# Kernel tuning notes

Hardware: AMD Instinct MI355X
Metric: run time of the kernel (lower is better)

The kernel has to match this reference:

```python
import jax, jax.numpy as jnp
import numpy as np

B, T, D = 32, 2048, 512

def setup_inputs() -> dict:
    key = jax.random.key(0)
    x = jax.random.normal(key, (B, T, D), dtype=jnp.float32)
    return {"x": x}

def reference(x) -> jnp.ndarray:
    # w[b,t] = sum_s <x_bt, x_bs> - <x_bt, x_bt>
    # Equivalent to x_bt . (sum_s x_bs) - ||x_bt||^2; avoids the [B,T,T] matrix.
    s = x.sum(axis=1)                                  # [B, D]
    w = jnp.einsum('btd,bd->bt', x, s) - (x * x).sum(axis=-1)  # [B, T]
    weights = jax.nn.softmax(w, axis=1)                # softmax over time
    # weighted pooling over time -> [B, D]
    representations = jnp.einsum('btd,bt->bd', x, weights)
    return representations
```

## Files before the change

kernel.cpp:

```cpp
#include <hip/hip_runtime.h>
#include <math.h>

constexpr int B = 32;
constexpr int T = 2048;
constexpr int D = 512;

constexpr int C1 = 32;
constexpr int R1 = T / C1;
constexpr int C2 = 128;
constexpr int RW = 4;
constexpr int NPART = C2;

__global__ __launch_bounds__(256) void colsum_part(const float* __restrict__ x,
                                                   float* __restrict__ P1) {
    const int b = blockIdx.x, c = blockIdx.y;
    const int d4 = threadIdx.x & 127;
    const int rp = threadIdx.x >> 7;
    const float4* xp = (const float4*)x + ((size_t)(b * T + c * R1) * D >> 2)
                       + (size_t)rp * (D / 4) + d4;
    float4 acc = {0.f, 0.f, 0.f, 0.f};
    #pragma unroll 8
    for (int i = 0; i < R1 / 2; ++i) {
        float4 v = xp[(size_t)i * (D / 2)];
        acc.x += v.x; acc.y += v.y; acc.z += v.z; acc.w += v.w;
    }
    __shared__ float4 lds[128];
    if (rp == 1) lds[d4] = acc;
    __syncthreads();
    if (rp == 0) {
        float4 o = lds[d4];
        acc.x += o.x; acc.y += o.y; acc.z += o.z; acc.w += o.w;
        ((float4*)P1)[(size_t)(b * C1 + c) * (D / 4) + d4] = acc;
    }
}

__global__ __launch_bounds__(256) void fused_pool(const float* __restrict__ x,
                                                  const float* __restrict__ P1,
                                                  float* __restrict__ Mp,
                                                  float* __restrict__ Sp,
                                                  float* __restrict__ Op) {
    const int b = blockIdx.x, c = blockIdx.y;
    const int tid = threadIdx.x, wid = tid >> 6, lane = tid & 63;

    __shared__ float  s_lds[D];
    __shared__ float  mred[4], sred[4];
    __shared__ float4 Obuf[4][D / 4];

    const int t0 = c * (4 * RW) + wid * RW;
    const float4* xr = (const float4*)(x + ((size_t)b * T + t0) * D) + lane * 2;
    float4 X0[RW], X1[RW];
    #pragma unroll
    for (int r = 0; r < RW; ++r) { X0[r] = xr[0]; X1[r] = xr[1]; xr += D / 4; }

    {
        const float2* pp = (const float2*)(P1 + (size_t)b * C1 * D) + tid;
        float2 acc = {0.f, 0.f};
        #pragma unroll
        for (int k = 0; k < C1; ++k) {
            float2 v = pp[(size_t)k * (D / 2)];
            acc.x += v.x; acc.y += v.y;
        }
        ((float2*)s_lds)[tid] = acc;
    }
    __syncthreads();
    const float4 s0 = ((const float4*)s_lds)[lane * 2];
    const float4 s1 = ((const float4*)s_lds)[lane * 2 + 1];

    float a[RW];
    #pragma unroll
    for (int r = 0; r < RW; ++r) {
        float t;
        t =      X0[r].x * (s0.x - X0[r].x);
        t = fmaf(X0[r].y,  s0.y - X0[r].y, t);
        t = fmaf(X0[r].z,  s0.z - X0[r].z, t);
        t = fmaf(X0[r].w,  s0.w - X0[r].w, t);
        t = fmaf(X1[r].x,  s1.x - X1[r].x, t);
        t = fmaf(X1[r].y,  s1.y - X1[r].y, t);
        t = fmaf(X1[r].z,  s1.z - X1[r].z, t);
        t = fmaf(X1[r].w,  s1.w - X1[r].w, t);
        a[r] = t;
    }
    #pragma unroll
    for (int off = 1; off < 64; off <<= 1) {
        #pragma unroll
        for (int r = 0; r < RW; ++r) a[r] += __shfl_xor(a[r], off, 64);
    }

    float m = fmaxf(fmaxf(a[0], a[1]), fmaxf(a[2], a[3]));
    float e[RW], ssum = 0.f;
    #pragma unroll
    for (int r = 0; r < RW; ++r) { e[r] = __expf(a[r] - m); ssum += e[r]; }

    float4 O0 = {0.f,0.f,0.f,0.f}, O1 = {0.f,0.f,0.f,0.f};
    #pragma unroll
    for (int r = 0; r < RW; ++r) {
        O0.x = fmaf(e[r], X0[r].x, O0.x); O0.y = fmaf(e[r], X0[r].y, O0.y);
        O0.z = fmaf(e[r], X0[r].z, O0.z); O0.w = fmaf(e[r], X0[r].w, O0.w);
        O1.x = fmaf(e[r], X1[r].x, O1.x); O1.y = fmaf(e[r], X1[r].y, O1.y);
        O1.z = fmaf(e[r], X1[r].z, O1.z); O1.w = fmaf(e[r], X1[r].w, O1.w);
    }

    if (lane == 0) { mred[wid] = m; sred[wid] = ssum; }
    __syncthreads();
    const float Mb = fmaxf(fmaxf(mred[0], mred[1]), fmaxf(mred[2], mred[3]));
    const float fw = __expf(m - Mb);
    Obuf[wid][lane * 2]     = make_float4(O0.x * fw, O0.y * fw, O0.z * fw, O0.w * fw);
    Obuf[wid][lane * 2 + 1] = make_float4(O1.x * fw, O1.y * fw, O1.z * fw, O1.w * fw);
    __syncthreads();
    if (tid == 0) {
        float Sb = sred[0] * __expf(mred[0] - Mb) + sred[1] * __expf(mred[1] - Mb)
                 + sred[2] * __expf(mred[2] - Mb) + sred[3] * __expf(mred[3] - Mb);
        Mp[b * C2 + c] = Mb;
        Sp[b * C2 + c] = Sb;
    }
    if (tid < D / 4) {
        float4 v0 = Obuf[0][tid], v1 = Obuf[1][tid], v2 = Obuf[2][tid], v3 = Obuf[3][tid];
        float4 r;
        r.x = (v0.x + v1.x) + (v2.x + v3.x);
        r.y = (v0.y + v1.y) + (v2.y + v3.y);
        r.z = (v0.z + v1.z) + (v2.z + v3.z);
        r.w = (v0.w + v1.w) + (v2.w + v3.w);
        ((float4*)Op)[(size_t)(b * C2 + c) * (D / 4) + tid] = r;
    }
}

__global__ __launch_bounds__(256) void merge_out(const float* __restrict__ Mp,
                                                 const float* __restrict__ Sp,
                                                 const float* __restrict__ Op,
                                                 float* __restrict__ out) {
    const int b = blockIdx.x;
    const int tid = threadIdx.x, wid = tid >> 6, lane = tid & 63;
    __shared__ float fmerge[NPART];
    __shared__ float red[4];
    __shared__ float misc[1];

    float Mc = -INFINITY, Sc = 0.f;
    if (tid < NPART) { Mc = Mp[b * NPART + tid]; Sc = Sp[b * NPART + tid]; }

    float mm = Mc;
    #pragma unroll
    for (int off = 1; off < 64; off <<= 1) mm = fmaxf(mm, __shfl_xor(mm, off, 64));
    if (lane == 0) red[wid] = mm;
    __syncthreads();
    const float Mg = fmaxf(fmaxf(red[0], red[1]), fmaxf(red[2], red[3]));
    __syncthreads();

    const float f = __expf(Mc - Mg);
    if (tid < NPART) fmerge[tid] = f;
    float fs = f * Sc;
    #pragma unroll
    for (int off = 1; off < 64; off <<= 1) fs += __shfl_xor(fs, off, 64);
    if (lane == 0) red[wid] = fs;
    __syncthreads();
    if (tid == 0) misc[0] = 1.0f / (red[0] + red[1] + red[2] + red[3]);
    __syncthreads();
    const float inv = misc[0];

    float2 acc = {0.f, 0.f};
    const float2* op = (const float2*)Op + (size_t)b * NPART * (D / 2) + tid;
    #pragma unroll 8
    for (int cc = 0; cc < NPART; ++cc) {
        const float fc = fmerge[cc];
        float2 v = op[(size_t)cc * (D / 2)];
        acc.x = fmaf(fc, v.x, acc.x);
        acc.y = fmaf(fc, v.y, acc.y);
    }
    ((float2*)out)[(size_t)b * (D / 2) + tid] = make_float2(acc.x * inv, acc.y * inv);
}

extern "C" void kernel_launch(void* const* d_in, const int* in_sizes, int n_in,
                              void* d_out, int out_size, void* d_ws, size_t ws_size,
                              hipStream_t stream) {
    const float* x = (const float*)d_in[0];
    float* out = (float*)d_out;

    float* P1 = (float*)d_ws;
    float* Mp = P1 + (size_t)B * C1 * D;
    float* Sp = Mp + (size_t)B * C2;
    float* Op = Sp + (size_t)B * C2;

    colsum_part<<<dim3(B, C1), 256, 0, stream>>>(x, P1);
    fused_pool<<<dim3(B, C2), 256, 0, stream>>>(x, P1, Mp, Sp, Op);
    merge_out<<<B, 256, 0, stream>>>(Mp, Sp, Op, out);
}
```

Baseline: 223.0 us.

## Process multiple row chunks per block with online softmax and register prefetch

Each wave now loops over several 4-row chunks and keeps a running max, sum and weighted accumulator in online-softmax style. The next chunk's rows are prefetched into registers while the current one is processed. Block count per batch drops by four, which reduces partial outputs, the redundant column-sum reduction per block and the merge work. The trade-off is fewer blocks in flight and a serial dependence across chunks, which could limit memory parallelism.

```diff
diff --git a/kernel.cpp b/kernel.cpp
--- a/kernel.cpp
+++ b/kernel.cpp
@@ -7,8 +7,10 @@
 
 constexpr int C1 = 32;
 constexpr int R1 = T / C1;
-constexpr int C2 = 128;
+constexpr int C2 = 32;
+constexpr int RPB = T / C2;
 constexpr int RW = 4;
+constexpr int NCHUNK = RPB / (4 * RW);
 constexpr int NPART = C2;
 
 __global__ __launch_bounds__(256) void colsum_part(const float* __restrict__ x,
@@ -46,7 +48,7 @@
     __shared__ float  mred[4], sred[4];
     __shared__ float4 Obuf[4][D / 4];
 
-    const int t0 = c * (4 * RW) + wid * RW;
+    const int t0 = c * RPB + wid * (NCHUNK * RW);
     const float4* xr = (const float4*)(x + ((size_t)b * T + t0) * D) + lane * 2;
     float4 X0[RW], X1[RW];
     #pragma unroll
@@ -66,38 +68,56 @@
     const float4 s0 = ((const float4*)s_lds)[lane * 2];
     const float4 s1 = ((const float4*)s_lds)[lane * 2 + 1];
 
-    float a[RW];
-    #pragma unroll
-    for (int r = 0; r < RW; ++r) {
-        float t;
-        t =      X0[r].x * (s0.x - X0[r].x);
-        t = fmaf(X0[r].y,  s0.y - X0[r].y, t);
-        t = fmaf(X0[r].z,  s0.z - X0[r].z, t);
-        t = fmaf(X0[r].w,  s0.w - X0[r].w, t);
-        t = fmaf(X1[r].x,  s1.x - X1[r].x, t);
-        t = fmaf(X1[r].y,  s1.y - X1[r].y, t);
-        t = fmaf(X1[r].z,  s1.z - X1[r].z, t);
-        t = fmaf(X1[r].w,  s1.w - X1[r].w, t);
-        a[r] = t;
-    }
-    #pragma unroll
-    for (int off = 1; off < 64; off <<= 1) {
-        #pragma unroll
-        for (int r = 0; r < RW; ++r) a[r] += __shfl_xor(a[r], off, 64);
-    }
-
-    float m = fmaxf(fmaxf(a[0], a[1]), fmaxf(a[2], a[3]));
-    float e[RW], ssum = 0.f;
-    #pragma unroll
-    for (int r = 0; r < RW; ++r) { e[r] = __expf(a[r] - m); ssum += e[r]; }
-
+    float m = -INFINITY, ssum = 0.f;
     float4 O0 = {0.f,0.f,0.f,0.f}, O1 = {0.f,0.f,0.f,0.f};
-    #pragma unroll
-    for (int r = 0; r < RW; ++r) {
-        O0.x = fmaf(e[r], X0[r].x, O0.x); O0.y = fmaf(e[r], X0[r].y, O0.y);
-        O0.z = fmaf(e[r], X0[r].z, O0.z); O0.w = fmaf(e[r], X0[r].w, O0.w);
-        O1.x = fmaf(e[r], X1[r].x, O1.x); O1.y = fmaf(e[r], X1[r].y, O1.y);
-        O1.z = fmaf(e[r], X1[r].z, O1.z); O1.w = fmaf(e[r], X1[r].w, O1.w);
+
+    #pragma unroll
+    for (int ch = 0; ch < NCHUNK; ++ch) {
+        float4 Y0[RW], Y1[RW];
+        #pragma unroll
+        for (int r = 0; r < RW; ++r) { Y0[r] = X0[r]; Y1[r] = X1[r]; }
+        if (ch + 1 < NCHUNK) {
+            #pragma unroll
+            for (int r = 0; r < RW; ++r) { X0[r] = xr[0]; X1[r] = xr[1]; xr += D / 4; }
+        }
+
+        float a[RW];
+        #pragma unroll
+        for (int r = 0; r < RW; ++r) {
+            float t;
+            t =      Y0[r].x * (s0.x - Y0[r].x);
+            t = fmaf(Y0[r].y,  s0.y - Y0[r].y, t);
+            t = fmaf(Y0[r].z,  s0.z - Y0[r].z, t);
+            t = fmaf(Y0[r].w,  s0.w - Y0[r].w, t);
+            t = fmaf(Y1[r].x,  s1.x - Y1[r].x, t);
+            t = fmaf(Y1[r].y,  s1.y - Y1[r].y, t);
+            t = fmaf(Y1[r].z,  s1.z - Y1[r].z, t);
+            t = fmaf(Y1[r].w,  s1.w - Y1[r].w, t);
+            a[r] = t;
+        }
+        #pragma unroll
+        for (int off = 1; off < 64; off <<= 1) {
+            #pragma unroll
+            for (int r = 0; r < RW; ++r) a[r] += __shfl_xor(a[r], off, 64);
+        }
+
+        const float mc = fmaxf(fmaxf(a[0], a[1]), fmaxf(a[2], a[3]));
+        const float mn = fmaxf(m, mc);
+        const float f  = __expf(m - mn);
+        float e[RW], es = 0.f;
+        #pragma unroll
+        for (int r = 0; r < RW; ++r) { e[r] = __expf(a[r] - mn); es += e[r]; }
+        ssum = fmaf(ssum, f, es);
+        O0.x *= f; O0.y *= f; O0.z *= f; O0.w *= f;
+        O1.x *= f; O1.y *= f; O1.z *= f; O1.w *= f;
+        #pragma unroll
+        for (int r = 0; r < RW; ++r) {
+            O0.x = fmaf(e[r], Y0[r].x, O0.x); O0.y = fmaf(e[r], Y0[r].y, O0.y);
+            O0.z = fmaf(e[r], Y0[r].z, O0.z); O0.w = fmaf(e[r], Y0[r].w, O0.w);
+            O1.x = fmaf(e[r], Y1[r].x, O1.x); O1.y = fmaf(e[r], Y1[r].y, O1.y);
+            O1.z = fmaf(e[r], Y1[r].z, O1.z); O1.w = fmaf(e[r], Y1[r].w, O1.w);
+        }
+        m = mn;
     }
 
     if (lane == 0) { mred[wid] = m; sred[wid] = ssum; }
```

New measurement: 219.5 us. About the same (-1.6%).
